# Performance work log

Hardware: AMD Instinct MI355X
Metric: run time of the kernel (lower is better)

Reference implementation:

```python
import jax, jax.numpy as jnp
import numpy as np

BS, K, FT = 256, 16, 512
HID = 256
EPS = 1e-5
SLOPE = 0.01  # LeakyReLU default negative slope


def setup_inputs() -> dict:
    key = jax.random.key(0)
    ks = jax.random.split(key, 6)
    cnn_output = jax.random.normal(ks[0], (BS, K, FT), dtype=jnp.float32)
    W1 = jax.random.normal(ks[1], (2 * FT, HID), dtype=jnp.float32) * (1.0 / np.sqrt(2 * FT))
    b1 = jnp.zeros((HID,), dtype=jnp.float32)
    gamma = jnp.ones((HID,), dtype=jnp.float32)
    beta = jnp.zeros((HID,), dtype=jnp.float32)
    W2 = jax.random.normal(ks[2], (HID, 1), dtype=jnp.float32) * (1.0 / np.sqrt(HID))
    b2 = jnp.zeros((1,), dtype=jnp.float32)
    return {"cnn_output": cnn_output, "W1": W1, "b1": b1, "gamma": gamma,
            "beta": beta, "W2": W2, "b2": b2}


def _aggregate_cat(cnn_output):
    bs, k, ft = cnn_output.shape
    iu, ju = jnp.triu_indices(k, k=1)          # pair order matches nested i<j loop
    p = iu.shape[0]
    shifts = (jnp.arange(p) % (bs - 1)) + 1    # 1,2,...,bs-1,1,2,...
    feat_i = jnp.transpose(cnn_output[:, iu], (1, 0, 2))  # [P, bs, ft]
    feat_j = jnp.transpose(cnn_output[:, ju], (1, 0, 2))  # [P, bs, ft]
    # roll(shift, dims=0)[b] == x[(b - shift) % bs]
    rows = (jnp.arange(bs)[None, :] - shifts[:, None]) % bs  # [P, bs]
    neg_j = cnn_output[rows, ju[:, None]]                    # [P, bs, ft]
    pos = jnp.concatenate([feat_i, feat_j], axis=-1).reshape(p * bs, 2 * ft)
    neg = jnp.concatenate([feat_i, neg_j], axis=-1).reshape(p * bs, 2 * ft)
    pairs = jnp.concatenate([pos, neg], axis=0)              # [2*P*bs, 2*ft]
    tgt = jnp.concatenate([jnp.ones((p * bs,), jnp.float32),
                           jnp.zeros((p * bs,), jnp.float32)])
    return pairs, tgt


def _relation_head(pairs, W1, b1, gamma, beta, W2, b2):
    h = pairs @ W1 + b1
    mean = jnp.mean(h, axis=0)
    var = jnp.var(h, axis=0)  # biased var, as torch BN in training mode
    hn = (h - mean) * jax.lax.rsqrt(var + EPS) * gamma + beta
    hn = jnp.where(hn >= 0, hn, SLOPE * hn)
    return (hn @ W2 + b2)[:, 0]


def _bce_with_logits(scores, tgt):
    # numerically stable BCEWithLogitsLoss (mean reduction)
    return jnp.mean(jnp.maximum(scores, 0.0) - scores * tgt
                    + jnp.log1p(jnp.exp(-jnp.abs(scores))))


def reference(cnn_output, W1, b1, gamma, beta, W2, b2):
    pairs, tgt = _aggregate_cat(cnn_output)
    scores = _relation_head(pairs, W1, b1, gamma, beta, W2, b2)
    loss = _bce_with_logits(scores, tgt)
    correct = jnp.stack([(scores > t / 10.0).astype(jnp.float32) == tgt
                         for t in range(1, 10)])  # [9, 2*P*bs] bool
    return loss, scores, correct
```

## Files before the change

### kernel.cpp

```cpp
#include <hip/hip_runtime.h>
#include <cmath>

#define KK 16
#define HID 256
#define NROWH 30720
#define NROW 61440
#define GM 4096
#define GK 512
#define GN 512
#define EPSV 1e-5f
#define SLOPEV 0.01f

#define BM 64
#define BN 32
#define BK 16
#define NT 32

__global__ __launch_bounds__(256) void k_gemm(const float* __restrict__ X,
                                              const float* __restrict__ W1,
                                              const float* __restrict__ b1,
                                              float* __restrict__ UV,
                                              float* __restrict__ sums8) {
  if (blockIdx.x == 0) {
    for (int i = threadIdx.x; i < 8 * 512 + 1; i += 256) sums8[i] = 0.0f;
  }
  __shared__ float As[2][BK][BM];
  __shared__ float Bs[2][BK][BN];
  const int id  = blockIdx.x;
  const int xcd = id & 7, wi = id >> 3;
  const int mt  = xcd * 8 + (wi >> 4);
  const int nt  = wi & 15;
  const int m0  = mt * BM, n0 = nt * BN;
  const float* Wb = (n0 < HID) ? (W1 + n0) : (W1 + GK * HID + (n0 - HID));
  const int t = threadIdx.x;
  const int arow = t >> 2;
  const int akq  = t & 3;
  const int brow = t >> 3;
  const int bcq  = t & 7;
  const int ty = t >> 4;
  const int tx = t & 15;

  const float* Xp = X + (size_t)m0 * GK;

  float4 ar, br;
  float acc[4][2] = {};

  auto stage = [&](int it) {
    ar = *(const float4*)(Xp + (size_t)arow * GK + it * BK + akq * 4);
    if (t < 128)
      br = *(const float4*)(Wb + (size_t)(it * BK + brow) * HID + bcq * 4);
  };
  auto write_lds = [&](int buf) {
    As[buf][akq * 4 + 0][arow] = ar.x;
    As[buf][akq * 4 + 1][arow] = ar.y;
    As[buf][akq * 4 + 2][arow] = ar.z;
    As[buf][akq * 4 + 3][arow] = ar.w;
    if (t < 128) *(float4*)&Bs[buf][brow][bcq * 4] = br;
  };

  stage(0);
  write_lds(0);
  __syncthreads();
  for (int it = 0; it < NT; ++it) {
    if (it + 1 < NT) stage(it + 1);
    const int buf = it & 1;
    #pragma unroll
    for (int kk = 0; kk < BK; ++kk) {
      float4 a = *(const float4*)&As[buf][kk][ty * 4];
      float2 b = *(const float2*)&Bs[buf][kk][tx * 2];
      float av[4] = {a.x, a.y, a.z, a.w};
      float bv[2] = {b.x, b.y};
      #pragma unroll
      for (int i = 0; i < 4; i++)
        #pragma unroll
        for (int j = 0; j < 2; j++)
          acc[i][j] = fmaf(av[i], bv[j], acc[i][j]);
    }
    if (it + 1 < NT) write_lds((it + 1) & 1);
    __syncthreads();
  }
  const int n = n0 + tx * 2;
  const float add0 = (n < HID) ? b1[n] : 0.0f;
  const float add1 = (n + 1 < HID) ? b1[n + 1] : 0.0f;
  #pragma unroll
  for (int i = 0; i < 4; i++) {
    const int m = m0 + ty * 4 + i;
    float2 v = {acc[i][0] + add0, acc[i][1] + add1};
    *(float2*)&UV[(size_t)m * GN + n] = v;
  }
}

__device__ __forceinline__ void decode_pair(int p, int& iu, int& ju) {
  int i = 0, q = p;
  while (q >= 15 - i) { q -= 15 - i; i++; }
  iu = i; ju = i + 1 + q;
}

__global__ __launch_bounds__(256) void k_stats(const float* __restrict__ UV,
                                               float* __restrict__ sums8) {
  const int bid = blockIdx.x;
  const int blk = (bid & 7) * 120 + (bid >> 3);
  const int p = blk >> 3;
  const int b0 = (blk & 7) * 32;
  const int f = threadIdx.x;
  int iu, ju; decode_pair(p, iu, ju);
  float s1 = 0.f, s2 = 0.f;
  for (int b = b0; b < b0 + 32; b++) {
    const int bi  = (b * KK + iu) * GN;
    const int bj1 = (b * KK + ju) * GN + HID;
    const int bj2 = (((b - p - 1) & 255) * KK + ju) * GN + HID;
    float u  = UV[bi + f];
    float h1 = u + UV[bj1 + f];
    float h2 = u + UV[bj2 + f];
    s1 += h1 + h2;
    s2 += h1 * h1 + h2 * h2;
  }
  float* dst = sums8 + (bid & 7) * 512;
  atomicAdd(dst + f, s1);
  atomicAdd(dst + 256 + f, s2);
}

__global__ __launch_bounds__(256) void k_finalize(const float* __restrict__ sums8,
                                                  const float* __restrict__ gamma,
                                                  const float* __restrict__ beta,
                                                  float* __restrict__ af,
                                                  float* __restrict__ cf) {
  const int f = threadIdx.x;
  float s1 = 0.f, s2 = 0.f;
  #pragma unroll
  for (int c = 0; c < 8; c++) {
    s1 += sums8[c * 512 + f];
    s2 += sums8[c * 512 + 256 + f];
  }
  float mean = s1 * (1.0f / NROW);
  float var  = s2 * (1.0f / NROW) - mean * mean;
  float a = gamma[f] * rsqrtf(var + EPSV);
  af[f] = a;
  cf[f] = beta[f] - mean * a;
}

__global__ __launch_bounds__(256) void k_scores(const float* __restrict__ UV,
                                                const float* __restrict__ af,
                                                const float* __restrict__ cf,
                                                const float* __restrict__ W2,
                                                const float* __restrict__ b2,
                                                float* __restrict__ out) {
  const int bid = blockIdx.x;
  const int swz = (bid & 7) * 960 + (bid >> 3);
  const int wv = swz * 4 + (threadIdx.x >> 6);
  const int lane = threadIdx.x & 63;
  const int p = wv >> 8, b = wv & 255;
  int iu, ju; decode_pair(p, iu, ju);
  const int bi  = (b * KK + iu) * GN;
  const int bj1 = (b * KK + ju) * GN + HID;
  const int bj2 = (((b - p - 1) & 255) * KK + ju) * GN + HID;
  float sp = 0.f, sn = 0.f;
  #pragma unroll
  for (int r = 0; r < 4; r++) {
    int f = lane + r * 64;
    float u = UV[bi + f];
    float a = af[f], c = cf[f], w = W2[f];
    float h1 = fmaf(a, u + UV[bj1 + f], c);
    h1 = h1 >= 0.f ? h1 : SLOPEV * h1;
    sp = fmaf(w, h1, sp);
    float h2 = fmaf(a, u + UV[bj2 + f], c);
    h2 = h2 >= 0.f ? h2 : SLOPEV * h2;
    sn = fmaf(w, h2, sn);
  }
  #pragma unroll
  for (int off = 32; off > 0; off >>= 1) {
    sp += __shfl_xor(sp, off, 64);
    sn += __shfl_xor(sn, off, 64);
  }
  if (lane == 0) {
    float bb = b2[0];
    out[1 + wv]         = sp + bb;
    out[1 + NROWH + wv] = sn + bb;
  }
}

__global__ __launch_bounds__(256) void k_bce(float* __restrict__ out,
                                             float* __restrict__ lossAcc) {
  const int row = blockIdx.x * 256 + threadIdx.x;
  float s = out[1 + row];
  const bool tgt = row < NROWH;
  float bce = fmaxf(s, 0.f) - (tgt ? s : 0.f) + log1pf(expf(-fabsf(s)));
  #pragma unroll
  for (int tt = 1; tt <= 9; tt++) {
    bool pred = (double)s > (double)tt / 10.0;
    out[1 + NROW + (tt - 1) * NROW + row] = (pred == tgt) ? 1.0f : 0.0f;
  }
  #pragma unroll
  for (int off = 32; off > 0; off >>= 1) bce += __shfl_xor(bce, off, 64);
  __shared__ float wsum[4];
  const int lane = threadIdx.x & 63, w = threadIdx.x >> 6;
  if (lane == 0) wsum[w] = bce;
  __syncthreads();
  if (threadIdx.x == 0) atomicAdd(lossAcc, wsum[0] + wsum[1] + wsum[2] + wsum[3]);
}

__global__ void k_loss(const float* __restrict__ lossAcc, float* __restrict__ out) {
  if (threadIdx.x == 0) out[0] = *lossAcc * (1.0f / NROW);
}

extern "C" void kernel_launch(void* const* d_in, const int* in_sizes, int n_in,
                              void* d_out, int out_size, void* d_ws, size_t ws_size,
                              hipStream_t stream) {
  const float* X     = (const float*)d_in[0];
  const float* W1    = (const float*)d_in[1];
  const float* b1    = (const float*)d_in[2];
  const float* gamma = (const float*)d_in[3];
  const float* beta  = (const float*)d_in[4];
  const float* W2    = (const float*)d_in[5];
  const float* b2    = (const float*)d_in[6];
  float* out = (float*)d_out;

  float* UV      = (float*)d_ws;
  float* sums8   = UV + (size_t)GM * GN;
  float* lossAcc = sums8 + 8 * 512;
  float* af      = lossAcc + 1;
  float* cf      = af + 256;

  hipLaunchKernelGGL(k_gemm,     dim3(1024), dim3(256), 0, stream, X, W1, b1, UV, sums8);
  hipLaunchKernelGGL(k_stats,    dim3(960),  dim3(256), 0, stream, UV, sums8);
  hipLaunchKernelGGL(k_finalize, dim3(1),    dim3(256), 0, stream, sums8, gamma, beta, af, cf);
  hipLaunchKernelGGL(k_scores,   dim3(7680), dim3(256), 0, stream, UV, af, cf, W2, b2, out);
  hipLaunchKernelGGL(k_bce,      dim3(240),  dim3(256), 0, stream, out, lossAcc);
  hipLaunchKernelGGL(k_loss,     dim3(1),    dim3(64),  0, stream, lossAcc, out);
}
```

Before: 142.1 us.

## Enlarge GEMM tiles, fuse BCE into scores kernel, spread loss atomics

The GEMM tile grows from 64x32 to 128x64, so each thread computes an 8x4 micro-tile and the grid drops to 256 blocks. This raises arithmetic intensity and cuts LDS and global traffic per FMA, but leaves fewer blocks to fill the CUs. The separate BCE kernel is folded into the scores kernel, so each block writes its 8 scores and thresholds directly and skips re-reading the scores from global memory. Loss accumulation goes to 64 padded slots that a single-wave kernel reduces, replacing one contended atomic and removing a launch.

```diff
diff --git a/kernel.cpp b/kernel.cpp
--- a/kernel.cpp
+++ b/kernel.cpp
@@ -11,8 +11,8 @@
 #define EPSV 1e-5f
 #define SLOPEV 0.01f
 
-#define BM 64
-#define BN 32
+#define BM 128
+#define BN 64
 #define BK 16
 #define NT 32
 
@@ -20,73 +20,76 @@
                                               const float* __restrict__ W1,
                                               const float* __restrict__ b1,
                                               float* __restrict__ UV,
-                                              float* __restrict__ sums8) {
+                                              float* __restrict__ zbuf) {
   if (blockIdx.x == 0) {
-    for (int i = threadIdx.x; i < 8 * 512 + 1; i += 256) sums8[i] = 0.0f;
+    for (int i = threadIdx.x; i < 5120; i += 256) zbuf[i] = 0.0f;
   }
   __shared__ float As[2][BK][BM];
   __shared__ float Bs[2][BK][BN];
-  const int id  = blockIdx.x;
-  const int xcd = id & 7, wi = id >> 3;
-  const int mt  = xcd * 8 + (wi >> 4);
-  const int nt  = wi & 15;
-  const int m0  = mt * BM, n0 = nt * BN;
+  const int id = blockIdx.x;
+  const int nt = id >> 5;
+  const int mt = id & 31;
+  const int m0 = mt * BM, n0 = nt * BN;
   const float* Wb = (n0 < HID) ? (W1 + n0) : (W1 + GK * HID + (n0 - HID));
   const int t = threadIdx.x;
-  const int arow = t >> 2;
-  const int akq  = t & 3;
-  const int brow = t >> 3;
-  const int bcq  = t & 7;
-  const int ty = t >> 4;
-  const int tx = t & 15;
-
-  const float* Xp = X + (size_t)m0 * GK;
-
-  float4 ar, br;
-  float acc[4][2] = {};
+  const int am  = t & 127;
+  const int ak8 = (t >> 7) * 8;
+  const int brr = t >> 4, bq = t & 15;
+  const int ty = t >> 4, tx = t & 15;
+
+  const float* Xp = X + (size_t)(m0 + am) * GK;
+
+  float4 a40, a41, b4;
+  float acc[8][4] = {};
 
   auto stage = [&](int it) {
-    ar = *(const float4*)(Xp + (size_t)arow * GK + it * BK + akq * 4);
-    if (t < 128)
-      br = *(const float4*)(Wb + (size_t)(it * BK + brow) * HID + bcq * 4);
+    const int k0 = it * BK + ak8;
+    a40 = *(const float4*)(Xp + k0);
+    a41 = *(const float4*)(Xp + k0 + 4);
+    b4  = *(const float4*)(Wb + (size_t)(it * BK + brr) * HID + bq * 4);
   };
-  auto write_lds = [&](int buf) {
-    As[buf][akq * 4 + 0][arow] = ar.x;
-    As[buf][akq * 4 + 1][arow] = ar.y;
-    As[buf][akq * 4 + 2][arow] = ar.z;
-    As[buf][akq * 4 + 3][arow] = ar.w;
-    if (t < 128) *(float4*)&Bs[buf][brow][bcq * 4] = br;
+  auto wr = [&](int buf) {
+    As[buf][ak8 + 0][am] = a40.x;
+    As[buf][ak8 + 1][am] = a40.y;
+    As[buf][ak8 + 2][am] = a40.z;
+    As[buf][ak8 + 3][am] = a40.w;
+    As[buf][ak8 + 4][am] = a41.x;
+    As[buf][ak8 + 5][am] = a41.y;
+    As[buf][ak8 + 6][am] = a41.z;
+    As[buf][ak8 + 7][am] = a41.w;
+    *(float4*)&Bs[buf][brr][bq * 4] = b4;
   };
 
   stage(0);
-  write_lds(0);
+  wr(0);
   __syncthreads();
   for (int it = 0; it < NT; ++it) {
     if (it + 1 < NT) stage(it + 1);
     const int buf = it & 1;
     #pragma unroll
     for (int kk = 0; kk < BK; ++kk) {
-      float4 a = *(const float4*)&As[buf][kk][ty * 4];
-      float2 b = *(const float2*)&Bs[buf][kk][tx * 2];
-      float av[4] = {a.x, a.y, a.z, a.w};
-      float bv[2] = {b.x, b.y};
+      float4 x0 = *(const float4*)&As[buf][kk][ty * 8];
+      float4 x1 = *(const float4*)&As[buf][kk][ty * 8 + 4];
+      float4 y  = *(const float4*)&Bs[buf][kk][tx * 4];
+      float av[8] = {x0.x, x0.y, x0.z, x0.w, x1.x, x1.y, x1.z, x1.w};
+      float bv[4] = {y.x, y.y, y.z, y.w};
       #pragma unroll
-      for (int i = 0; i < 4; i++)
+      for (int i = 0; i < 8; i++)
         #pragma unroll
-        for (int j = 0; j < 2; j++)
+        for (int j = 0; j < 4; j++)
           acc[i][j] = fmaf(av[i], bv[j], acc[i][j]);
     }
-    if (it + 1 < NT) write_lds((it + 1) & 1);
+    if (it + 1 < NT) wr((it + 1) & 1);
     __syncthreads();
   }
-  const int n = n0 + tx * 2;
-  const float add0 = (n < HID) ? b1[n] : 0.0f;
-  const float add1 = (n + 1 < HID) ? b1[n + 1] : 0.0f;
-  #pragma unroll
-  for (int i = 0; i < 4; i++) {
-    const int m = m0 + ty * 4 + i;
-    float2 v = {acc[i][0] + add0, acc[i][1] + add1};
-    *(float2*)&UV[(size_t)m * GN + n] = v;
+  const int n = n0 + tx * 4;
+  float4 add = {0.f, 0.f, 0.f, 0.f};
+  if (n < HID) add = *(const float4*)&b1[n];
+  #pragma unroll
+  for (int i = 0; i < 8; i++) {
+    const int m = m0 + ty * 8 + i;
+    float4 v = {acc[i][0] + add.x, acc[i][1] + add.y, acc[i][2] + add.z, acc[i][3] + add.w};
+    *(float4*)&UV[(size_t)m * GN + n] = v;
   }
 }
 
@@ -144,11 +147,14 @@
                                                 const float* __restrict__ cf,
                                                 const float* __restrict__ W2,
                                                 const float* __restrict__ b2,
-                                                float* __restrict__ out) {
+                                                float* __restrict__ out,
+                                                float* __restrict__ lossAcc64) {
   const int bid = blockIdx.x;
   const int swz = (bid & 7) * 960 + (bid >> 3);
-  const int wv = swz * 4 + (threadIdx.x >> 6);
+  const int wv0 = swz * 4;
+  const int w = threadIdx.x >> 6;
   const int lane = threadIdx.x & 63;
+  const int wv = wv0 + w;
   const int p = wv >> 8, b = wv & 255;
   int iu, ju; decode_pair(p, iu, ju);
   const int bi  = (b * KK + iu) * GN;
@@ -159,48 +165,56 @@
   for (int r = 0; r < 4; r++) {
     int f = lane + r * 64;
     float u = UV[bi + f];
-    float a = af[f], c = cf[f], w = W2[f];
+    float a = af[f], c = cf[f], ww = W2[f];
     float h1 = fmaf(a, u + UV[bj1 + f], c);
     h1 = h1 >= 0.f ? h1 : SLOPEV * h1;
-    sp = fmaf(w, h1, sp);
+    sp = fmaf(ww, h1, sp);
     float h2 = fmaf(a, u + UV[bj2 + f], c);
     h2 = h2 >= 0.f ? h2 : SLOPEV * h2;
-    sn = fmaf(w, h2, sn);
+    sn = fmaf(ww, h2, sn);
   }
   #pragma unroll
   for (int off = 32; off > 0; off >>= 1) {
     sp += __shfl_xor(sp, off, 64);
     sn += __shfl_xor(sn, off, 64);
   }
+  __shared__ float sc[8];
+  __shared__ float sbce[8];
   if (lane == 0) {
     float bb = b2[0];
-    out[1 + wv]         = sp + bb;
-    out[1 + NROWH + wv] = sn + bb;
-  }
-}
-
-__global__ __launch_bounds__(256) void k_bce(float* __restrict__ out,
-                                             float* __restrict__ lossAcc) {
-  const int row = blockIdx.x * 256 + threadIdx.x;
-  float s = out[1 + row];
-  const bool tgt = row < NROWH;
-  float bce = fmaxf(s, 0.f) - (tgt ? s : 0.f) + log1pf(expf(-fabsf(s)));
-  #pragma unroll
-  for (int tt = 1; tt <= 9; tt++) {
-    bool pred = (double)s > (double)tt / 10.0;
-    out[1 + NROW + (tt - 1) * NROW + row] = (pred == tgt) ? 1.0f : 0.0f;
-  }
-  #pragma unroll
-  for (int off = 32; off > 0; off >>= 1) bce += __shfl_xor(bce, off, 64);
-  __shared__ float wsum[4];
-  const int lane = threadIdx.x & 63, w = threadIdx.x >> 6;
-  if (lane == 0) wsum[w] = bce;
+    sc[w]     = sp + bb;
+    sc[4 + w] = sn + bb;
+  }
   __syncthreads();
-  if (threadIdx.x == 0) atomicAdd(lossAcc, wsum[0] + wsum[1] + wsum[2] + wsum[3]);
-}
-
-__global__ void k_loss(const float* __restrict__ lossAcc, float* __restrict__ out) {
-  if (threadIdx.x == 0) out[0] = *lossAcc * (1.0f / NROW);
+  const int t = threadIdx.x;
+  if (t < 8) {
+    const int j = t & 3;
+    const bool pos = t < 4;
+    const int row = (pos ? 0 : NROWH) + wv0 + j;
+    const float s = sc[t];
+    out[1 + row] = s;
+    float bce = fmaxf(s, 0.f) - (pos ? s : 0.f) + log1pf(expf(-fabsf(s)));
+    sbce[t] = bce;
+    #pragma unroll
+    for (int tt = 1; tt <= 9; tt++) {
+      bool pred = (double)s > (double)tt / 10.0;
+      out[1 + NROW + (tt - 1) * NROW + row] = (pred == pos) ? 1.0f : 0.0f;
+    }
+  }
+  __syncthreads();
+  if (t == 0) {
+    float bsum = sbce[0] + sbce[1] + sbce[2] + sbce[3]
+               + sbce[4] + sbce[5] + sbce[6] + sbce[7];
+    atomicAdd(&lossAcc64[(bid & 63) * 16], bsum);
+  }
+}
+
+__global__ void k_loss(const float* __restrict__ lossAcc64, float* __restrict__ out) {
+  const int t = threadIdx.x;
+  float v = lossAcc64[t * 16];
+  #pragma unroll
+  for (int off = 32; off > 0; off >>= 1) v += __shfl_xor(v, off, 64);
+  if (t == 0) out[0] = v * (1.0f / NROW);
 }
 
 extern "C" void kernel_launch(void* const* d_in, const int* in_sizes, int n_in,
@@ -215,16 +229,15 @@
   const float* b2    = (const float*)d_in[6];
   float* out = (float*)d_out;
 
-  float* UV      = (float*)d_ws;
-  float* sums8   = UV + (size_t)GM * GN;
-  float* lossAcc = sums8 + 8 * 512;
-  float* af      = lossAcc + 1;
-  float* cf      = af + 256;
-
-  hipLaunchKernelGGL(k_gemm,     dim3(1024), dim3(256), 0, stream, X, W1, b1, UV, sums8);
+  float* UV        = (float*)d_ws;
+  float* sums8     = UV + (size_t)GM * GN;
+  float* lossAcc64 = sums8 + 8 * 512;
+  float* af        = lossAcc64 + 1024;
+  float* cf        = af + 256;
+
+  hipLaunchKernelGGL(k_gemm,     dim3(256),  dim3(256), 0, stream, X, W1, b1, UV, sums8);
   hipLaunchKernelGGL(k_stats,    dim3(960),  dim3(256), 0, stream, UV, sums8);
   hipLaunchKernelGGL(k_finalize, dim3(1),    dim3(256), 0, stream, sums8, gamma, beta, af, cf);
-  hipLaunchKernelGGL(k_scores,   dim3(7680), dim3(256), 0, stream, UV, af, cf, W2, b2, out);
-  hipLaunchKernelGGL(k_bce,      dim3(240),  dim3(256), 0, stream, out, lossAcc);
-  hipLaunchKernelGGL(k_loss,     dim3(1),    dim3(64),  0, stream, lossAcc, out);
-}
+  hipLaunchKernelGGL(k_scores,   dim3(7680), dim3(256), 0, stream, UV, af, cf, W2, b2, out, lossAcc64);
+  hipLaunchKernelGGL(k_loss,     dim3(1),    dim3(64),  0, stream, lossAcc64, out);
+}
```

New measurement: 131.9 us. 1.08x faster.
